# Kernel optimization log

Measured on AMD Instinct MI355X. Metric: run time of the kernel, lower is better.

Reference implementation:

```python
import jax, jax.numpy as jnp
import numpy as np

B, S, DIM = 4, 2048, 2048
H, KVH, HD = 32, 8, 64
REPEATS = H // KVH
SCALE = HD ** -0.5


def _rope(x, cos, sin):
    # x: (B, S, Hn, HD); cos/sin: (S, HD//2)
    xr = x[..., 0::2]
    xi = x[..., 1::2]
    c = cos[:, None, :]  # (S, 1, HD//2) broadcasts over heads
    s = sin[:, None, :]
    out_r = xr * c - xi * s
    out_i = xr * s + xi * c
    return jnp.stack([out_r, out_i], axis=-1).reshape(x.shape)


def setup_inputs() -> dict:
    key = jax.random.key(0)
    ks = jax.random.split(key, 5)
    x = jax.random.normal(ks[0], (B, S, DIM), dtype=jnp.float32)
    wq = jax.random.normal(ks[1], (H * HD, DIM), dtype=jnp.float32) * 0.02
    wk = jax.random.normal(ks[2], (KVH * HD, DIM), dtype=jnp.float32) * 0.02
    wv = jax.random.normal(ks[3], (KVH * HD, DIM), dtype=jnp.float32) * 0.02
    wo = jax.random.normal(ks[4], (DIM, H * HD), dtype=jnp.float32) * 0.02
    # standard RoPE frequencies: freqs_cis = exp(i * t * theta)
    inv_freq = 1.0 / (10000.0 ** (jnp.arange(0, HD, 2, dtype=jnp.float32) / HD))
    angles = jnp.arange(S, dtype=jnp.float32)[:, None] * inv_freq[None, :]  # (S, HD//2)
    return {
        "x": x, "wq": wq, "wk": wk, "wv": wv, "wo": wo,
        "freqs_cos": jnp.cos(angles), "freqs_sin": jnp.sin(angles),
    }


def reference(x, wq, wk, wv, wo, freqs_cos, freqs_sin):
    b, s, _ = x.shape
    q = (x @ wq.T).reshape(b, s, H, HD)
    k = (x @ wk.T).reshape(b, s, KVH, HD)
    v = (x @ wv.T).reshape(b, s, KVH, HD)
    q = _rope(q, freqs_cos, freqs_sin)
    k = _rope(k, freqs_cos, freqs_sin)
    k_rep = jnp.repeat(k, REPEATS, axis=2)  # (B,S,H,HD)
    v_rep = jnp.repeat(v, REPEATS, axis=2)
    # NOTE: faithful to source - q is NOT transposed to (B,H,S,HD), so the
    # matmul contracts head_dim at each token, producing (B,S,H,H) scores
    # (mixing across heads per position), softmaxed over the last head axis.
    scores = jnp.einsum('bshd,bsed->bshe', q, k_rep) * SCALE  # (B,S,H,H)
    weights = jax.nn.softmax(scores, axis=-1)
    out = jnp.einsum('bshe,bsed->bshd', weights, v_rep)  # (B,S,H,HD)
    out = out.reshape(b, s, H * HD)
    return out @ wo.T
```

## Files before the change

kernel.cpp:

```cpp
#include <hip/hip_runtime.h>

typedef unsigned short u16;
typedef __bf16 bf16x8 __attribute__((ext_vector_type(8)));
typedef float f32x4 __attribute__((ext_vector_type(4)));

#define AS1 __attribute__((address_space(1)))
#define AS3 __attribute__((address_space(3)))

__device__ inline u16 f2bf(float f) {
    union { float f; unsigned u; } c; c.f = f;
    unsigned u = c.u;
    u += 0x7fffu + ((u >> 16) & 1u);
    return (u16)(u >> 16);
}
__device__ inline float bf2f(u16 b) {
    union { unsigned u; float f; } c; c.u = ((unsigned)b) << 16;
    return c.f;
}

__device__ inline void async_cp16(const void* g, void* l) {
    __builtin_amdgcn_global_load_lds((const AS1 void*)g, (AS3 void*)l, 16, 0, 0);
}

__global__ __launch_bounds__(256)
void conv_all(const float* __restrict__ x,
              const float* __restrict__ wq, const float* __restrict__ wk,
              const float* __restrict__ wv, const float* __restrict__ wo,
              u16* __restrict__ x_bf, u16* __restrict__ wqkv,
              u16* __restrict__ wo_bf) {
    int b = blockIdx.x;
    if (b < 8192) {
        int i = (b * 256 + threadIdx.x) * 8;
        float4 f0 = *(const float4*)(x + i);
        float4 f1 = *(const float4*)(x + i + 4);
        union { u16 h[8]; uint4 v; } o;
        o.h[0] = f2bf(f0.x); o.h[1] = f2bf(f0.y);
        o.h[2] = f2bf(f0.z); o.h[3] = f2bf(f0.w);
        o.h[4] = f2bf(f1.x); o.h[5] = f2bf(f1.y);
        o.h[6] = f2bf(f1.z); o.h[7] = f2bf(f1.w);
        *(uint4*)(x_bf + i) = o.v;
    } else {
        int i = ((b - 8192) * 256 + threadIdx.x) * 4;
        const float* src;
        u16* dst;
        if (i < 4194304)       { src = wq + i;           dst = wqkv + i; }
        else if (i < 5242880)  { src = wk + (i-4194304); dst = wqkv + i; }
        else if (i < 6291456)  { src = wv + (i-5242880); dst = wqkv + i; }
        else                   { src = wo + (i-6291456); dst = wo_bf + (i-6291456); }
        float4 f = *(const float4*)src;
        union { u16 h[4]; uint2 v; } o;
        o.h[0] = f2bf(f.x); o.h[1] = f2bf(f.y);
        o.h[2] = f2bf(f.z); o.h[3] = f2bf(f.w);
        *(uint2*)dst = o.v;
    }
}

template <int NI, bool BF16_OUT>
__global__ __launch_bounds__(512, 2)
void gemm_bt8(const u16* __restrict__ A, const u16* __restrict__ B,
              void* __restrict__ Cout, int N, int K) {
    constexpr int SZ = 32768 + NI * 8192;
    __shared__ __align__(16) char ldsc[2 * SZ];

    const int tid  = threadIdx.x;
    const int w    = tid >> 6;
    const int lane = tid & 63;
    const int row0 = blockIdx.x * 256;
    const int col0 = blockIdx.y * (NI * 64);
    const int wm = w >> 2, wn = w & 3;
    const int lm = lane & 15, quad = lane >> 4;

    const int NT  = K / 64;
    const int NIT = K / 128;
    const int K64 = K * 64;

    const int sr  = lane >> 3;
    const int stC = ((lane & 7) ^ sr) * 8;
    const u16* pA = A + (size_t)(row0 + w * 8 + sr) * K + stC;
    const u16* pB = B + (size_t)(col0 + w * 8 + sr) * K + stC;
    const int stagoff = w * 1024;

    const int cx0   = (quad ^ (lm & 7)) * 16;
    const int cx1   = cx0 ^ 64;
    const int aBase = (wm * 128 + lm) * 128;
    const int bBase = 32768 + (wn * (NI * 16) + lm) * 128;

    f32x4 acc[8][NI];
#pragma unroll
    for (int i = 0; i < 8; i++)
#pragma unroll
        for (int j = 0; j < NI; j++) acc[i][j] = (f32x4){0.f, 0.f, 0.f, 0.f};

    auto stage = [&](const u16* base, int v, int unit, int regionOff) {
        int kb = (v < NT ? v : NT - 1) * 64;
        async_cp16(base + (size_t)unit * K64 + kb,
                   ldsc + (v & 1) * SZ + regionOff + unit * 8192 + stagoff);
    };
#define ST_A(v, u) stage(pA, (v), (u), 0)
#define ST_B(v, u) stage(pB, (v), (u), 32768)

#define LDR(off) (*(const bf16x8*)(ldsc + (off)))
#define SB __builtin_amdgcn_sched_barrier(0)
#define BAR __builtin_amdgcn_s_barrier()
#define WLG(n) asm volatile("s_waitcnt lgkmcnt(" #n ")" ::: "memory")

#define RD_AF(DST, BASEOFF, MIBASE)                                           \
    _Pragma("unroll")                                                         \
    for (int j = 0; j < 2; j++) {                                             \
        DST[j][0] = LDR((BASEOFF) + aBase + ((MIBASE) + j) * 2048 + cx0);     \
        DST[j][1] = LDR((BASEOFF) + aBase + ((MIBASE) + j) * 2048 + cx1);     \
    }
#define RD_BG(DST, BASEOFF)                                                   \
    _Pragma("unroll")                                                         \
    for (int ni = 0; ni < NI; ni++) {                                         \
        DST[ni][0] = LDR((BASEOFF) + bBase + ni * 2048 + cx0);                \
        DST[ni][1] = LDR((BASEOFF) + bBase + ni * 2048 + cx1);                \
    }
#define MFMA_TAIL(MI0, AF, BG)                                                \
    __builtin_amdgcn_s_setprio(1);                                            \
    _Pragma("unroll")                                                         \
    for (int s = 0; s < 2; s++)                                               \
        _Pragma("unroll")                                                     \
        for (int j = 0; j < 2; j++)                                           \
            _Pragma("unroll")                                                 \
            for (int ni = 0; ni < NI; ni++)                                   \
                acc[(MI0) + j][ni] = __builtin_amdgcn_mfma_f32_16x16x32_bf16( \
                    AF[j][s], BG[ni][s], acc[(MI0) + j][ni], 0, 0, 0);        \
    __builtin_amdgcn_s_setprio(0);

    bf16x8 bgA[NI][2], bgB[NI][2], F[2][2], G[2][2];

#pragma unroll
    for (int u = 0; u < 4; u++) ST_A(0, u);
#pragma unroll
    for (int u = 0; u < NI; u++) ST_B(0, u);
#pragma unroll
    for (int u = 0; u < NI; u++) ST_B(1, u);
    ST_A(1, 0);
    if constexpr (NI == 3) asm volatile("s_waitcnt vmcnt(4)" ::: "memory");
    else                   asm volatile("s_waitcnt vmcnt(5)" ::: "memory");
    SB;
    if constexpr (NI == 3) { RD_BG(bgA, 0) }
    RD_AF(F, 0, 0)
    SB;
    BAR;

#define HALF_ITER(u, BO, BN, BGC, BGN)                                        \
    {                                                                         \
                                                                      \
        if constexpr (NI == 4) { RD_BG(BGC, BO) }                             \
        SB;                                                                   \
        RD_AF(G, BO, 2)                                                       \
        SB;                                                                   \
        ST_A((u) + 1, 1); ST_A((u) + 1, 2); ST_A((u) + 1, 3);                 \
        SB;                                                                   \
        BAR;                                                                  \
        WLG(4);                                                               \
        SB;                                                                   \
        MFMA_TAIL(0, F, BGC)                                                  \
        SB;                                                                   \
        BAR;                                                                  \
                                                                      \
        RD_AF(F, BO, 4)                                                       \
        SB;                                                                   \
        ST_B((u) + 2, 0); ST_B((u) + 2, 1);                                   \
        SB;                                                                   \
        BAR;                                                                  \
        WLG(4);                                                               \
        SB;                                                                   \
        MFMA_TAIL(2, G, BGC)                                                  \
        SB;                                                                   \
        BAR;                                                                  \
                                                                      \
        RD_AF(G, BO, 6)                                                       \
        SB;                                                                   \
        ST_B((u) + 2, 2);                                                     \
        if constexpr (NI == 4) { ST_B((u) + 2, 3); }                          \
        ST_A((u) + 2, 0);                                                     \
        SB;                                                                   \
        BAR;                                                                  \
        WLG(4);                                                               \
        SB;                                                                   \
        MFMA_TAIL(4, F, BGC)                                                  \
        SB;                                                                   \
        BAR;                                                                  \
                               \
        WLG(0);                                                               \
        SB;                                                                   \
        MFMA_TAIL(6, G, BGC)                                                  \
        SB;                                                                   \
        if constexpr (NI == 3) asm volatile("s_waitcnt vmcnt(4)" ::: "memory");\
        else                   asm volatile("s_waitcnt vmcnt(5)" ::: "memory");\
        SB;                                                                   \
        if constexpr (NI == 3) { RD_BG(BGN, BN) }                             \
        RD_AF(F, BN, 0)                                                       \
        SB;                                                                   \
        BAR;                                                                  \
    }

    for (int it = 0; it < NIT; ++it) {
        const int t = 2 * it;
        HALF_ITER(t, 0, SZ, bgA, bgB)
        HALF_ITER(t + 1, SZ, 0, bgB, bgA)
    }

#undef HALF_ITER
#undef MFMA_TAIL
#undef RD_BG
#undef RD_AF
#undef WLG
#undef BAR
#undef SB
#undef LDR
#undef ST_A
#undef ST_B

    const int rbase = row0 + wm * 128 + quad * 4;
    const int cbase = col0 + wn * (NI * 16) + lm;
    if (BF16_OUT) {
        u16* C = (u16*)Cout;
#pragma unroll
        for (int mi = 0; mi < 8; mi++)
#pragma unroll
            for (int r = 0; r < 4; r++) {
                size_t ro = (size_t)(rbase + mi * 16 + r) * N;
#pragma unroll
                for (int ni = 0; ni < NI; ni++)
                    C[ro + cbase + ni * 16] = f2bf(acc[mi][ni][r]);
            }
    } else {
        float* C = (float*)Cout;
#pragma unroll
        for (int mi = 0; mi < 8; mi++)
#pragma unroll
            for (int r = 0; r < 4; r++) {
                size_t ro = (size_t)(rbase + mi * 16 + r) * N;
#pragma unroll
                for (int ni = 0; ni < NI; ni++)
                    C[ro + cbase + ni * 16] = acc[mi][ni][r];
            }
    }
}

__global__ __launch_bounds__(256)
void attn_tok(const u16* __restrict__ qkv, u16* __restrict__ out) {
    __shared__ float kvf[1024];
    const int tok = blockIdx.x;
    const int t = threadIdx.x;
    const u16* qrow = qkv + (size_t)tok * 3072;

    {
        uint2 w = *(const uint2*)(qrow + 2048 + t * 4);
        kvf[t * 4 + 0] = bf2f((u16)(w.x & 0xffff));
        kvf[t * 4 + 1] = bf2f((u16)(w.x >> 16));
        kvf[t * 4 + 2] = bf2f((u16)(w.y & 0xffff));
        kvf[t * 4 + 3] = bf2f((u16)(w.y >> 16));
    }
    __syncthreads();

    const int h = t >> 3, j = t & 7;
    float qf[8];
    {
        uint4 w = *(const uint4*)(qrow + h * 64 + j * 8);
        unsigned ws4[4] = {w.x, w.y, w.z, w.w};
#pragma unroll
        for (int i = 0; i < 4; i++) {
            qf[2 * i]     = bf2f((u16)(ws4[i] & 0xffff));
            qf[2 * i + 1] = bf2f((u16)(ws4[i] >> 16));
        }
    }

    float s[8];
#pragma unroll
    for (int g = 0; g < 8; g++) {
        const float4* kk = (const float4*)(kvf + g * 64 + j * 8);
        float4 k0 = kk[0], k1 = kk[1];
        s[g] = qf[0] * k0.x + qf[1] * k0.y + qf[2] * k0.z + qf[3] * k0.w
             + qf[4] * k1.x + qf[5] * k1.y + qf[6] * k1.z + qf[7] * k1.w;
    }
#pragma unroll
    for (int g = 0; g < 8; g++) {
        s[g] += __shfl_xor(s[g], 1);
        s[g] += __shfl_xor(s[g], 2);
        s[g] += __shfl_xor(s[g], 4);
    }
    float m = -1e30f;
#pragma unroll
    for (int g = 0; g < 8; g++) { s[g] *= 0.125f; m = fmaxf(m, s[g]); }
    float p[8], l = 0.f;
#pragma unroll
    for (int g = 0; g < 8; g++) { p[g] = __expf(s[g] - m); l += p[g]; }
    float rl = 1.f / l;

    float o[8] = {0, 0, 0, 0, 0, 0, 0, 0};
#pragma unroll
    for (int g = 0; g < 8; g++) {
        float wgt = p[g] * rl;
        const float4* vv = (const float4*)(kvf + 512 + g * 64 + j * 8);
        float4 v0 = vv[0], v1 = vv[1];
        o[0] += wgt * v0.x; o[1] += wgt * v0.y;
        o[2] += wgt * v0.z; o[3] += wgt * v0.w;
        o[4] += wgt * v1.x; o[5] += wgt * v1.y;
        o[6] += wgt * v1.z; o[7] += wgt * v1.w;
    }

    unsigned po[4];
#pragma unroll
    for (int i = 0; i < 4; i++)
        po[i] = (unsigned)f2bf(o[2 * i]) | ((unsigned)f2bf(o[2 * i + 1]) << 16);
    uint4 wo_; wo_.x = po[0]; wo_.y = po[1]; wo_.z = po[2]; wo_.w = po[3];
    *(uint4*)(out + (size_t)tok * 2048 + h * 64 + j * 8) = wo_;
}

extern "C" void kernel_launch(void* const* d_in, const int* in_sizes, int n_in,
                              void* d_out, int out_size, void* d_ws, size_t ws_size,
                              hipStream_t stream) {
    const float* x  = (const float*)d_in[0];
    const float* wq = (const float*)d_in[1];
    const float* wk = (const float*)d_in[2];
    const float* wv = (const float*)d_in[3];
    const float* wo = (const float*)d_in[4];

    u16* x_bf  = (u16*)d_ws;
    u16* wqkv  = x_bf  + 16777216;
    u16* wo_bf = wqkv  + 6291456;
    u16* qkv   = wo_bf + 4194304;
    u16* attn  = x_bf;

    conv_all<<<18432, dim3(256), 0, stream>>>(x, wq, wk, wv, wo, x_bf, wqkv, wo_bf);

    gemm_bt8<3, true><<<dim3(32, 16), dim3(512), 0, stream>>>(x_bf, wqkv, qkv,
                                                              3072, 2048);

    attn_tok<<<8192, dim3(256), 0, stream>>>(qkv, attn);

    gemm_bt8<4, false><<<dim3(32, 8), dim3(512), 0, stream>>>(attn, wo_bf,
                                                              (float*)d_out,
                                                              2048, 2048);
}
```

Before: 320.5 us.

## Replace eight-phase GEMM pipeline with simpler two-phase per-tile schedule

Reworks the main loop of both bf16 GEMMs. The old schedule interleaved fine-grained LDS reads, async global-to-LDS copies and MFMA groups across four barrier-separated phases per k-tile. The new one reads the full half-k fragments for all 8 M-subtiles at once, issues every async copy for tile u+2 in a single batch, and runs two long MFMA trains with fewer barriers. This aims to cut barrier and scheduling overhead and lengthen uninterrupted MFMA runs, at the cost of more live fragment registers and coarser overlap of memory traffic with compute, which could hurt occupancy at the two-blocks-per-CU launch bound.

```diff
diff --git a/kernel.cpp b/kernel.cpp
--- a/kernel.cpp
+++ b/kernel.cpp
@@ -57,7 +57,7 @@
 
 template <int NI, bool BF16_OUT>
 __global__ __launch_bounds__(512, 2)
-void gemm_bt8(const u16* __restrict__ A, const u16* __restrict__ B,
+void gemm_bt2(const u16* __restrict__ A, const u16* __restrict__ B,
               void* __restrict__ Cout, int N, int K) {
     constexpr int SZ = 32768 + NI * 8192;
     __shared__ __align__(16) char ldsc[2 * SZ];
@@ -96,124 +96,96 @@
         async_cp16(base + (size_t)unit * K64 + kb,
                    ldsc + (v & 1) * SZ + regionOff + unit * 8192 + stagoff);
     };
-#define ST_A(v, u) stage(pA, (v), (u), 0)
-#define ST_B(v, u) stage(pB, (v), (u), 32768)
+#define ST_ALL(v)                                                             \
+    {                                                                         \
+        _Pragma("unroll")                                                     \
+        for (int uu = 0; uu < 4; uu++) stage(pA, (v), uu, 0);                 \
+        _Pragma("unroll")                                                     \
+        for (int uu = 0; uu < NI; uu++) stage(pB, (v), uu, 32768);            \
+    }
 
 #define LDR(off) (*(const bf16x8*)(ldsc + (off)))
 #define SB __builtin_amdgcn_sched_barrier(0)
 #define BAR __builtin_amdgcn_s_barrier()
-#define WLG(n) asm volatile("s_waitcnt lgkmcnt(" #n ")" ::: "memory")
-
-#define RD_AF(DST, BASEOFF, MIBASE)                                           \
-    _Pragma("unroll")                                                         \
-    for (int j = 0; j < 2; j++) {                                             \
-        DST[j][0] = LDR((BASEOFF) + aBase + ((MIBASE) + j) * 2048 + cx0);     \
-        DST[j][1] = LDR((BASEOFF) + aBase + ((MIBASE) + j) * 2048 + cx1);     \
-    }
-#define RD_BG(DST, BASEOFF)                                                   \
-    _Pragma("unroll")                                                         \
-    for (int ni = 0; ni < NI; ni++) {                                         \
-        DST[ni][0] = LDR((BASEOFF) + bBase + ni * 2048 + cx0);                \
-        DST[ni][1] = LDR((BASEOFF) + bBase + ni * 2048 + cx1);                \
-    }
-#define MFMA_TAIL(MI0, AF, BG)                                                \
+#define WLG0 asm volatile("s_waitcnt lgkmcnt(0)" ::: "memory")
+#define WLG_S1INFLIGHT                                                        \
+    do {                                                                      \
+        if constexpr (NI == 3)                                                \
+            asm volatile("s_waitcnt lgkmcnt(11)" ::: "memory");               \
+        else                                                                  \
+            asm volatile("s_waitcnt lgkmcnt(12)" ::: "memory");               \
+    } while (0)
+#define VMC                                                                   \
+    do {                                                                      \
+        if constexpr (NI == 3)                                                \
+            asm volatile("s_waitcnt vmcnt(7)" ::: "memory");                  \
+        else                                                                  \
+            asm volatile("s_waitcnt vmcnt(8)" ::: "memory");                  \
+    } while (0)
+
+#define RD_HALF(S, BO, CXV)                                                   \
+    {                                                                         \
+        _Pragma("unroll")                                                     \
+        for (int ni = 0; ni < NI; ni++)                                       \
+            bgs[S][ni] = LDR((BO) + bBase + ni * 2048 + (CXV));               \
+        _Pragma("unroll")                                                     \
+        for (int mi = 0; mi < 8; mi++)                                        \
+            af[S][mi] = LDR((BO) + aBase + mi * 2048 + (CXV));                \
+    }
+#define MFMA_TRAIN(S)                                                         \
     __builtin_amdgcn_s_setprio(1);                                            \
     _Pragma("unroll")                                                         \
-    for (int s = 0; s < 2; s++)                                               \
-        _Pragma("unroll")                                                     \
-        for (int j = 0; j < 2; j++)                                           \
-            _Pragma("unroll")                                                 \
-            for (int ni = 0; ni < NI; ni++)                                   \
-                acc[(MI0) + j][ni] = __builtin_amdgcn_mfma_f32_16x16x32_bf16( \
-                    AF[j][s], BG[ni][s], acc[(MI0) + j][ni], 0, 0, 0);        \
+    for (int mi = 0; mi < 8; mi++)                                            \
+        _Pragma("unroll")                                                     \
+        for (int ni = 0; ni < NI; ni++)                                       \
+            acc[mi][ni] = __builtin_amdgcn_mfma_f32_16x16x32_bf16(            \
+                af[S][mi], bgs[S][ni], acc[mi][ni], 0, 0, 0);                 \
     __builtin_amdgcn_s_setprio(0);
 
-    bf16x8 bgA[NI][2], bgB[NI][2], F[2][2], G[2][2];
-
-#pragma unroll
-    for (int u = 0; u < 4; u++) ST_A(0, u);
-#pragma unroll
-    for (int u = 0; u < NI; u++) ST_B(0, u);
-#pragma unroll
-    for (int u = 0; u < NI; u++) ST_B(1, u);
-    ST_A(1, 0);
-    if constexpr (NI == 3) asm volatile("s_waitcnt vmcnt(4)" ::: "memory");
-    else                   asm volatile("s_waitcnt vmcnt(5)" ::: "memory");
-    SB;
-    if constexpr (NI == 3) { RD_BG(bgA, 0) }
-    RD_AF(F, 0, 0)
-    SB;
+    bf16x8 bgs[2][NI], af[2][8];
+
+    ST_ALL(0)
+    ST_ALL(1)
+    VMC;
     BAR;
 
-#define HALF_ITER(u, BO, BN, BGC, BGN)                                        \
+#define TILE(u, BO)                                                           \
     {                                                                         \
-                                                                      \
-        if constexpr (NI == 4) { RD_BG(BGC, BO) }                             \
-        SB;                                                                   \
-        RD_AF(G, BO, 2)                                                       \
-        SB;                                                                   \
-        ST_A((u) + 1, 1); ST_A((u) + 1, 2); ST_A((u) + 1, 3);                 \
+        RD_HALF(0, BO, cx0)                                                   \
+        SB;                                                                   \
+        RD_HALF(1, BO, cx1)                                                   \
+        SB;                                                                   \
+        WLG_S1INFLIGHT;                                                       \
+        SB;                                                                   \
+        MFMA_TRAIN(0)                                                         \
+        SB;                                                                   \
+        WLG0;                                                                 \
         SB;                                                                   \
         BAR;                                                                  \
-        WLG(4);                                                               \
-        SB;                                                                   \
-        MFMA_TAIL(0, F, BGC)                                                  \
-        SB;                                                                   \
-        BAR;                                                                  \
-                                                                      \
-        RD_AF(F, BO, 4)                                                       \
-        SB;                                                                   \
-        ST_B((u) + 2, 0); ST_B((u) + 2, 1);                                   \
-        SB;                                                                   \
-        BAR;                                                                  \
-        WLG(4);                                                               \
-        SB;                                                                   \
-        MFMA_TAIL(2, G, BGC)                                                  \
-        SB;                                                                   \
-        BAR;                                                                  \
-                                                                      \
-        RD_AF(G, BO, 6)                                                       \
-        SB;                                                                   \
-        ST_B((u) + 2, 2);                                                     \
-        if constexpr (NI == 4) { ST_B((u) + 2, 3); }                          \
-        ST_A((u) + 2, 0);                                                     \
-        SB;                                                                   \
-        BAR;                                                                  \
-        WLG(4);                                                               \
-        SB;                                                                   \
-        MFMA_TAIL(4, F, BGC)                                                  \
-        SB;                                                                   \
-        BAR;                                                                  \
-                               \
-        WLG(0);                                                               \
-        SB;                                                                   \
-        MFMA_TAIL(6, G, BGC)                                                  \
-        SB;                                                                   \
-        if constexpr (NI == 3) asm volatile("s_waitcnt vmcnt(4)" ::: "memory");\
-        else                   asm volatile("s_waitcnt vmcnt(5)" ::: "memory");\
-        SB;                                                                   \
-        if constexpr (NI == 3) { RD_BG(BGN, BN) }                             \
-        RD_AF(F, BN, 0)                                                       \
-        SB;                                                                   \
+        ST_ALL((u) + 2)                                                       \
+        SB;                                                                   \
+        MFMA_TRAIN(1)                                                         \
+        SB;                                                                   \
+        VMC;                                                                  \
         BAR;                                                                  \
     }
 
     for (int it = 0; it < NIT; ++it) {
         const int t = 2 * it;
-        HALF_ITER(t, 0, SZ, bgA, bgB)
-        HALF_ITER(t + 1, SZ, 0, bgB, bgA)
-    }
-
-#undef HALF_ITER
-#undef MFMA_TAIL
-#undef RD_BG
-#undef RD_AF
-#undef WLG
+        TILE(t, 0)
+        TILE(t + 1, SZ)
+    }
+
+#undef TILE
+#undef MFMA_TRAIN
+#undef RD_HALF
+#undef VMC
+#undef WLG_S1INFLIGHT
+#undef WLG0
 #undef BAR
 #undef SB
 #undef LDR
-#undef ST_A
-#undef ST_B
+#undef ST_ALL
 
     const int rbase = row0 + wm * 128 + quad * 4;
     const int cbase = col0 + wn * (NI * 16) + lm;
@@ -329,12 +301,12 @@
 
     conv_all<<<18432, dim3(256), 0, stream>>>(x, wq, wk, wv, wo, x_bf, wqkv, wo_bf);
 
-    gemm_bt8<3, true><<<dim3(32, 16), dim3(512), 0, stream>>>(x_bf, wqkv, qkv,
+    gemm_bt2<3, true><<<dim3(32, 16), dim3(512), 0, stream>>>(x_bf, wqkv, qkv,
                                                               3072, 2048);
 
     attn_tok<<<8192, dim3(256), 0, stream>>>(qkv, attn);
 
-    gemm_bt8<4, false><<<dim3(32, 8), dim3(512), 0, stream>>>(attn, wo_bf,
+    gemm_bt2<4, false><<<dim3(32, 8), dim3(512), 0, stream>>>(attn, wo_bf,
                                                               (float*)d_out,
                                                               2048, 2048);
 }
```

Measured after the change: 323.2 us. No clear change (+0.8%).
